# Kernel tuning notes

Hardware: AMD Instinct MI355X
Metric: run time of the kernel (lower is better)

Reference implementation:

```python
import jax, jax.numpy as jnp
import numpy as np

D_CONV = 4
D_STATE = 16
DT_RANK = 64


def _silu(x):
    return x * jax.nn.sigmoid(x)


def setup_inputs() -> dict:
    key = jax.random.key(0)
    ks = jax.random.split(key, 10)
    B, L, dim = 2, 1024, 1024
    d_inner = 2 * dim
    s = lambda fan: 1.0 / np.sqrt(fan)
    inp = {
        "x": jax.random.normal(ks[0], (B, L, dim), jnp.float32),
        "ln_w": jnp.ones((dim,), jnp.float32),
        "ln_b": jnp.zeros((dim,), jnp.float32),
        "w_in": jax.random.normal(ks[1], (2 * d_inner, dim), jnp.float32) * s(dim),
        "conv_w": jax.random.normal(ks[2], (d_inner, D_CONV), jnp.float32) * s(D_CONV),
        "conv_b": jnp.zeros((d_inner,), jnp.float32),
        "w_xproj": jax.random.normal(ks[3], (DT_RANK + 2 * D_STATE, d_inner), jnp.float32) * s(d_inner),
        "w_dt": jax.random.normal(ks[4], (d_inner, DT_RANK), jnp.float32) * s(DT_RANK),
        "b_dt": jax.random.normal(ks[5], (d_inner,), jnp.float32) * 0.1,
        # S4D-real init: A = -(1..d_state) per channel
        "a_log": jnp.tile(jnp.log(jnp.arange(1, D_STATE + 1, dtype=jnp.float32)), (d_inner, 1)),
        "d_skip": jnp.ones((d_inner,), jnp.float32),
        "w_out": jax.random.normal(ks[6], (dim, d_inner), jnp.float32) * s(d_inner),
    }
    return inp


def reference(x, ln_w, ln_b, w_in, conv_w, conv_b, w_xproj, w_dt, b_dt, a_log, d_skip, w_out):
    B, L, dim = x.shape
    residual = x

    # LayerNorm
    mu = jnp.mean(x, axis=-1, keepdims=True)
    var = jnp.mean((x - mu) ** 2, axis=-1, keepdims=True)
    xn = (x - mu) * jax.lax.rsqrt(var + 1e-5) * ln_w + ln_b

    # in_proj -> (x_ssm, z) each (B, L, d_inner)
    xz = jnp.einsum("bld,ed->ble", xn, w_in)
    d_inner = xz.shape[-1] // 2
    xs, z = xz[..., :d_inner], xz[..., d_inner:]

    # depthwise causal conv1d (kernel D_CONV) + SiLU
    xp = jnp.pad(xs, ((0, 0), (D_CONV - 1, 0), (0, 0)))
    xc = conv_b
    for k in range(D_CONV):
        xc = xc + conv_w[:, k] * xp[:, k : k + L, :]
    u = _silu(xc)  # (B, L, d_inner)

    # x_proj -> dt, B, C
    x_dbl = jnp.einsum("ble,re->blr", u, w_xproj)
    dt_r = x_dbl[..., :DT_RANK]
    B_ssm = x_dbl[..., DT_RANK : DT_RANK + D_STATE]         # (B, L, n)
    C_ssm = x_dbl[..., DT_RANK + D_STATE :]                 # (B, L, n)

    dt = jax.nn.softplus(jnp.einsum("blr,er->ble", dt_r, w_dt) + b_dt)  # (B, L, d_inner)

    A = -jnp.exp(a_log)  # (d_inner, n)
    deltaA = jnp.exp(jnp.einsum("ble,en->blen", dt, A))            # (B, L, e, n)
    deltaBu = jnp.einsum("ble,bln,ble->blen", dt, B_ssm, u)        # (B, L, e, n)

    # selective scan over L
    def step(h, ins):
        dA_t, dBu_t, C_t = ins
        h = dA_t * h + dBu_t                       # (B, e, n)
        y = jnp.einsum("ben,bn->be", h, C_t)
        return h, y

    h0 = jnp.zeros((B, d_inner, D_STATE), xs.dtype)
    _, ys = jax.lax.scan(
        step,
        h0,
        (deltaA.transpose(1, 0, 2, 3), deltaBu.transpose(1, 0, 2, 3), C_ssm.transpose(1, 0, 2)),
    )
    y = ys.transpose(1, 0, 2) + u * d_skip         # (B, L, e)

    y = y * _silu(z)
    out = jnp.einsum("ble,de->bld", y, w_out)
    return residual + out
```

## Files before the change

kernel.cpp:

```cpp
#include <hip/hip_runtime.h>
#include <hip/hip_bf16.h>


#define LC 16
#define NCHUNK 64

typedef short bf16x8 __attribute__((ext_vector_type(8)));
typedef float f32x4  __attribute__((ext_vector_type(4)));

static __device__ __forceinline__ float siluf(float x) { return x / (1.f + __expf(-x)); }
static __device__ __forceinline__ unsigned short f2bf(float f) {
    unsigned int u = __float_as_uint(f);
    unsigned int r = (u + 0x7fffu + ((u >> 16) & 1u)) >> 16;
    return (unsigned short)r;
}
static __device__ __forceinline__ float bfb(unsigned short u) {
    return __uint_as_float(((unsigned int)u) << 16);
}
static __device__ __forceinline__ void gload_lds16(const void* g, void* l) {
    __builtin_amdgcn_global_load_lds(
        (const __attribute__((address_space(1))) void*)g,
        (__attribute__((address_space(3))) void*)l, 16, 0, 0);
}

__global__ __launch_bounds__(256) void setup_kernel(
    const float* __restrict__ w_in,  unsigned short* __restrict__ w_in_b,
    const float* __restrict__ w_out, unsigned short* __restrict__ w_out_b,
    const float* __restrict__ w_dt,  unsigned short* __restrict__ w_dt_b,
    const float* __restrict__ x,
    const float* __restrict__ ln_w,
    const float* __restrict__ ln_b,
    unsigned short* __restrict__ xn)
{
    int bid = blockIdx.x, tid = threadIdx.x;
    if (bid < 6272) {
        int i = bid * 256 + tid;
        const float* in; unsigned short* outp; int j;
        if (i < 1048576)      { in = w_in;  outp = w_in_b;  j = i; }
        else if (i < 1572864) { in = w_out; outp = w_out_b; j = i - 1048576; }
        else if (i < 1605632) { in = w_dt;  outp = w_dt_b;  j = i - 1572864; }
        else return;
        float4 v = reinterpret_cast<const float4*>(in)[j];
        ushort4 o = { f2bf(v.x), f2bf(v.y), f2bf(v.z), f2bf(v.w) };
        reinterpret_cast<ushort4*>(outp)[j] = o;
        return;
    }
    int m = bid - 6272;
    const float4* xr = reinterpret_cast<const float4*>(x) + (size_t)m * 256;
    float4 r = xr[tid];
    float f0 = r.x, f1 = r.y, f2 = r.z, f3 = r.w;
    float s  = f0 + f1 + f2 + f3;
    float s2 = f0*f0 + f1*f1 + f2*f2 + f3*f3;
    #pragma unroll
    for (int off = 32; off > 0; off >>= 1) {
        s  += __shfl_down(s, off);
        s2 += __shfl_down(s2, off);
    }
    __shared__ float red[8];
    if ((tid & 63) == 0) { red[tid >> 6] = s; red[4 + (tid >> 6)] = s2; }
    __syncthreads();
    float st = red[0] + red[1] + red[2] + red[3];
    float qt = red[4] + red[5] + red[6] + red[7];
    float mu   = st * (1.f / 1024.f);
    float var  = qt * (1.f / 1024.f) - mu * mu;
    float rstd = rsqrtf(var + 1e-5f);
    float4 wv = reinterpret_cast<const float4*>(ln_w)[tid];
    float4 bv = reinterpret_cast<const float4*>(ln_b)[tid];
    ushort4 o = { f2bf((f0 - mu) * rstd * wv.x + bv.x),
                  f2bf((f1 - mu) * rstd * wv.y + bv.y),
                  f2bf((f2 - mu) * rstd * wv.z + bv.z),
                  f2bf((f3 - mu) * rstd * wv.w + bv.w) };
    reinterpret_cast<ushort4*>(xn + (size_t)m * 1024)[tid] = o;
}

__global__ __launch_bounds__(256) void gemm_bf16_nt(
    const unsigned short* __restrict__ A, int lda,
    const unsigned short* __restrict__ B, int ldb,
    int Kslice,
    float* __restrict__ C, unsigned short* __restrict__ Cb, int ldc,
    int ep, size_t Cstride)
{
    __shared__ short As[3 * 64 * 32];
    __shared__ short Bs[3 * 128 * 32];
    int tid = threadIdx.x;
    int z = blockIdx.z;
    A += (size_t)z * Kslice;
    B += (size_t)z * Kslice;
    C += (size_t)z * Cstride;

    int gx = gridDim.x;
    int wg = blockIdx.y * gx + blockIdx.x;
    int nwg = gx * gridDim.y;
    int cpx = nwg >> 3;
    int swz = (wg & 7) * cpx + (wg >> 3);
    int bx = swz % gx, by = swz / gx;

    int m0 = by * 64, n0 = bx * 128;
    int lane = tid & 63, wave = tid >> 6;
    int wm = (wave >> 1) * 32, wn = (wave & 1) * 64;
    int frow = lane & 15, fq = lane >> 4;

    f32x4 acc[2][4] = {};

    int lrow = lane >> 2;
    int scol = (lane & 3) * 8;
    const unsigned short* AgL = A + (size_t)(m0 + wave * 16 + lrow) * lda + scol;
    const unsigned short* BgL = B + (size_t)(n0 + wave * 16 + lrow) * ldb + scol;
    int aoff = (wave * 16) * 32;
    int boff = (wave * 16) * 32;

    #pragma unroll
    for (int p = 0; p < 2; ++p) {
        int nk = p * 32;
        gload_lds16(AgL + nk,                    As + p * 2048 + aoff);
        gload_lds16(BgL + nk,                    Bs + p * 4096 + boff);
        gload_lds16(BgL + (size_t)64 * ldb + nk, Bs + p * 4096 + boff + 64 * 32);
    }

    int cur = 0;
    for (int k0 = 0; k0 < Kslice; k0 += 32) {
        if (k0 + 32 < Kslice) {
            asm volatile("s_waitcnt vmcnt(3) lgkmcnt(0)" ::: "memory");
        } else {
            asm volatile("s_waitcnt vmcnt(0) lgkmcnt(0)" ::: "memory");
        }
        __builtin_amdgcn_s_barrier();
        int nk = k0 + 64;
        if (nk < Kslice) {
            int stg = cur - 1; if (stg < 0) stg = 2;
            gload_lds16(AgL + nk,                    As + stg * 2048 + aoff);
            gload_lds16(BgL + nk,                    Bs + stg * 4096 + boff);
            gload_lds16(BgL + (size_t)64 * ldb + nk, Bs + stg * 4096 + boff + 64 * 32);
        }
        const short* Ac = As + cur * 2048;
        const short* Bc = Bs + cur * 4096;
        bf16x8 af[2], bfr[4];
        #pragma unroll
        for (int i = 0; i < 2; ++i)
            af[i] = *reinterpret_cast<const bf16x8*>(Ac + (wm + i * 16 + frow) * 32 + fq * 8);
        #pragma unroll
        for (int j = 0; j < 4; ++j)
            bfr[j] = *reinterpret_cast<const bf16x8*>(Bc + (wn + j * 16 + frow) * 32 + fq * 8);
        #pragma unroll
        for (int i = 0; i < 2; ++i)
            #pragma unroll
            for (int j = 0; j < 4; ++j)
                acc[i][j] = __builtin_amdgcn_mfma_f32_16x16x32_bf16(af[i], bfr[j], acc[i][j], 0, 0, 0);
        cur = (cur == 2) ? 0 : cur + 1;
    }

    int cn = lane & 15, rq = (lane >> 4) * 4;
    #pragma unroll
    for (int i = 0; i < 2; ++i) {
        #pragma unroll
        for (int j = 0; j < 4; ++j) {
            #pragma unroll
            for (int r = 0; r < 4; ++r) {
                int row = m0 + wm + i * 16 + rq + r;
                int col = n0 + wn + j * 16 + cn;
                float v = acc[i][j][r];
                if (ep == 0) {
                    C[(size_t)row * ldc + col] = v;
                } else {
                    Cb[(size_t)row * ldc + col] = f2bf(v);
                }
            }
        }
    }
}

__global__ __launch_bounds__(256) void out_reduce(
    const float* __restrict__ part, const float* __restrict__ x,
    float* __restrict__ out)
{
    int i = blockIdx.x * 256 + threadIdx.x;
    float4 s = reinterpret_cast<const float4*>(x)[i];
    #pragma unroll
    for (int z = 0; z < 4; ++z) {
        float4 p = reinterpret_cast<const float4*>(part + (size_t)z * 2097152)[i];
        s.x += p.x; s.y += p.y; s.z += p.z; s.w += p.w;
    }
    reinterpret_cast<float4*>(out)[i] = s;
}

__global__ __launch_bounds__(256) void xproj_splitk(
    const unsigned short* __restrict__ xz,
    const float* __restrict__ cw,
    const float* __restrict__ cb,
    const float* __restrict__ B,
    unsigned short* __restrict__ u,
    float* __restrict__ part)
{
    __shared__ float As[16][68];
    __shared__ float Bs[16][100];
    int tid = threadIdx.x;
    int m0 = blockIdx.x * 64;
    int k0 = blockIdx.y * 64;
    int tx = tid & 15;
    int ty = tid >> 4;
    float acc[4][6] = {};
    int arow = tid >> 2, akg = (tid & 3) << 2;
    int brow1 = (256 + tid) >> 2, bkg1 = ((256 + tid) & 3) << 2;
    int m = m0 + arow;
    int l = m & 1023;

    for (int ks = 0; ks < 64; ks += 16) {
        int e0 = k0 + ks + akg;
        float xv[4][4];
        #pragma unroll
        for (int kk = 0; kk < 4; ++kk) {
            ushort4 t = make_ushort4(0, 0, 0, 0);
            if (l - 3 + kk >= 0)
                t = *reinterpret_cast<const ushort4*>(xz + (size_t)(m - 3 + kk) * 4096 + e0);
            xv[kk][0] = bfb(t.x); xv[kk][1] = bfb(t.y);
            xv[kk][2] = bfb(t.z); xv[kk][3] = bfb(t.w);
        }
        float4 cbv = *reinterpret_cast<const float4*>(cb + e0);
        float cbs[4] = { cbv.x, cbv.y, cbv.z, cbv.w };
        float res[4];
        #pragma unroll
        for (int j = 0; j < 4; ++j) {
            float4 w = *reinterpret_cast<const float4*>(cw + (size_t)(e0 + j) * 4);
            float a = cbs[j];
            a = fmaf(w.x, xv[0][j], a);
            a = fmaf(w.y, xv[1][j], a);
            a = fmaf(w.z, xv[2][j], a);
            a = fmaf(w.w, xv[3][j], a);
            res[j] = siluf(a);
        }
        ushort4 uo = { f2bf(res[0]), f2bf(res[1]), f2bf(res[2]), f2bf(res[3]) };
        *reinterpret_cast<ushort4*>(u + (size_t)m * 2048 + e0) = uo;

        float4 bv0 = make_float4(0.f, 0.f, 0.f, 0.f), bv1 = bv0;
        if (arow < 96)  bv0 = *reinterpret_cast<const float4*>(B + (size_t)arow * 2048 + k0 + ks + akg);
        if (brow1 < 96) bv1 = *reinterpret_cast<const float4*>(B + (size_t)brow1 * 2048 + k0 + ks + bkg1);
        __syncthreads();
        As[akg + 0][arow] = res[0]; As[akg + 1][arow] = res[1];
        As[akg + 2][arow] = res[2]; As[akg + 3][arow] = res[3];
        if (arow < 96) {
            Bs[akg + 0][arow] = bv0.x; Bs[akg + 1][arow] = bv0.y;
            Bs[akg + 2][arow] = bv0.z; Bs[akg + 3][arow] = bv0.w;
        }
        if (brow1 < 96) {
            Bs[bkg1 + 0][brow1] = bv1.x; Bs[bkg1 + 1][brow1] = bv1.y;
            Bs[bkg1 + 2][brow1] = bv1.z; Bs[bkg1 + 3][brow1] = bv1.w;
        }
        __syncthreads();
        #pragma unroll
        for (int k = 0; k < 16; ++k) {
            float aa[4], bb[6];
            #pragma unroll
            for (int i = 0; i < 4; ++i) aa[i] = As[k][ty * 4 + i];
            #pragma unroll
            for (int j = 0; j < 6; ++j) bb[j] = Bs[k][tx * 6 + j];
            #pragma unroll
            for (int i = 0; i < 4; ++i)
                #pragma unroll
                for (int j = 0; j < 6; ++j)
                    acc[i][j] = fmaf(aa[i], bb[j], acc[i][j]);
        }
    }
    float* p = part + (size_t)blockIdx.y * 196608;
    #pragma unroll
    for (int i = 0; i < 4; ++i)
        #pragma unroll
        for (int j = 0; j < 6; ++j)
            p[(size_t)(m0 + ty * 4 + i) * 96 + tx * 6 + j] = acc[i][j];
}

__global__ __launch_bounds__(256) void xproj_reduce(
    const float* __restrict__ part, float* __restrict__ xdbl)
{
    int i = blockIdx.x * 256 + threadIdx.x;
    float s = 0.f;
    #pragma unroll
    for (int sd = 0; sd < 32; ++sd) s += part[(size_t)sd * 196608 + i];
    xdbl[i] = s;
}

static __device__ __forceinline__ void dt_tile256(
    const float* __restrict__ xdbl, const unsigned short* __restrict__ w_dt_b,
    const float* __restrict__ b_dt, size_t rbase, int et,
    int lane, int wave, float dtl[LC][256])
{
    int frow = lane & 15, fq = lane >> 4;
    bf16x8 af[2];
    #pragma unroll
    for (int kk = 0; kk < 2; ++kk) {
        const float* ap = xdbl + (rbase + frow) * 96 + kk * 32 + fq * 8;
        float4 a0 = *reinterpret_cast<const float4*>(ap);
        float4 a1 = *reinterpret_cast<const float4*>(ap + 4);
        bf16x8 t;
        t[0] = (short)f2bf(a0.x); t[1] = (short)f2bf(a0.y);
        t[2] = (short)f2bf(a0.z); t[3] = (short)f2bf(a0.w);
        t[4] = (short)f2bf(a1.x); t[5] = (short)f2bf(a1.y);
        t[6] = (short)f2bf(a1.z); t[7] = (short)f2bf(a1.w);
        af[kk] = t;
    }
    f32x4 dacc[4] = {};
    #pragma unroll
    for (int j = 0; j < 4; ++j)
        #pragma unroll
        for (int kk = 0; kk < 2; ++kk) {
            int row_e = et * 256 + wave * 64 + j * 16 + frow;
            bf16x8 bfr = *reinterpret_cast<const bf16x8*>(
                w_dt_b + (size_t)row_e * 64 + kk * 32 + fq * 8);
            dacc[j] = __builtin_amdgcn_mfma_f32_16x16x32_bf16(af[kk], bfr, dacc[j], 0, 0, 0);
        }
    int cn = lane & 15, rq = (lane >> 4) * 4;
    #pragma unroll
    for (int j = 0; j < 4; ++j)
        #pragma unroll
        for (int r = 0; r < 4; ++r) {
            int lrow = rq + r;
            int ecol = wave * 64 + j * 16 + cn;
            float v = dacc[j][r] + b_dt[et * 256 + ecol];
            v = (v > 20.f) ? v : log1pf(__expf(v));
            dtl[lrow][ecol] = bfb(f2bf(v));
        }
}

__global__ __launch_bounds__(256) void scan_part1(
    const unsigned short* __restrict__ u,
    const float* __restrict__ xdbl,
    const unsigned short* __restrict__ w_dt_b,
    const float* __restrict__ b_dt,
    const float* __restrict__ a_log,
    float* __restrict__ hpart,
    float* __restrict__ Aprod)
{
    __shared__ float dtl[LC][256];
    int tid = threadIdx.x;
    int lane = tid & 63, wave = tid >> 6;
    int bid = blockIdx.x;
    int c = bid & 63, et = (bid >> 6) & 7, b = bid >> 9;
    int e = et * 256 + tid;
    size_t rbase = (size_t)b * 1024 + c * LC;

    dt_tile256(xdbl, w_dt_b, b_dt, rbase, et, lane, wave, dtl);

    float A[16];
    #pragma unroll
    for (int q = 0; q < 4; ++q) {
        float4 al = *reinterpret_cast<const float4*>(a_log + (size_t)e * 16 + q * 4);
        A[q * 4 + 0] = -__expf(al.x); A[q * 4 + 1] = -__expf(al.y);
        A[q * 4 + 2] = -__expf(al.z); A[q * 4 + 3] = -__expf(al.w);
    }
    float h[16], P[16];
    #pragma unroll
    for (int n = 0; n < 16; ++n) { h[n] = 0.f; P[n] = 1.f; }

    const unsigned short* u_p = u + rbase * 2048 + e;
    const float* b_p = xdbl + rbase * 96 + 64;
    __syncthreads();
    #pragma unroll
    for (int l = 0; l < LC; ++l) {
        float dtv = dtl[l][tid];
        float u_c = bfb(u_p[(size_t)l * 2048]);
        float Bv[16];
        #pragma unroll
        for (int q = 0; q < 4; ++q) {
            float4 bv = *reinterpret_cast<const float4*>(b_p + (size_t)l * 96 + q * 4);
            Bv[q * 4 + 0] = bv.x; Bv[q * 4 + 1] = bv.y;
            Bv[q * 4 + 2] = bv.z; Bv[q * 4 + 3] = bv.w;
        }
        float du = dtv * u_c;
        #pragma unroll
        for (int n = 0; n < 16; ++n) {
            float d = __expf(dtv * A[n]);
            h[n] = fmaf(d, h[n], du * Bv[n]);
            P[n] *= d;
        }
    }
    size_t oidx = (size_t)c * 65536 + ((size_t)b * 2048 + e) * 16;
    #pragma unroll
    for (int q = 0; q < 4; ++q) {
        *reinterpret_cast<float4*>(hpart + oidx + q * 4) =
            make_float4(h[q * 4], h[q * 4 + 1], h[q * 4 + 2], h[q * 4 + 3]);
        *reinterpret_cast<float4*>(Aprod + oidx + q * 4) =
            make_float4(P[q * 4], P[q * 4 + 1], P[q * 4 + 2], P[q * 4 + 3]);
    }
}

__global__ __launch_bounds__(256) void scan_combine(
    const float* __restrict__ hpart,
    const float* __restrict__ Aprod,
    float* __restrict__ hinit)
{
    int t = blockIdx.x * 256 + threadIdx.x;
    float h = 0.f;
    #pragma unroll 8
    for (int c = 0; c < NCHUNK; ++c) {
        hinit[(size_t)c * 65536 + t] = h;
        float P  = Aprod[(size_t)c * 65536 + t];
        float hp = hpart[(size_t)c * 65536 + t];
        h = fmaf(P, h, hp);
    }
}

__global__ __launch_bounds__(256) void scan_part2(
    const unsigned short* __restrict__ u,
    const float* __restrict__ xdbl,
    const unsigned short* __restrict__ w_dt_b,
    const float* __restrict__ b_dt,
    const unsigned short* __restrict__ xz,
    const float* __restrict__ a_log,
    const float* __restrict__ d_skip,
    const float* __restrict__ hinit,
    unsigned short* __restrict__ y)
{
    __shared__ float dtl[LC][256];
    int tid = threadIdx.x;
    int lane = tid & 63, wave = tid >> 6;
    int bid = blockIdx.x;
    int c = bid & 63, et = (bid >> 6) & 7, b = bid >> 9;
    int e = et * 256 + tid;
    size_t rbase = (size_t)b * 1024 + c * LC;

    dt_tile256(xdbl, w_dt_b, b_dt, rbase, et, lane, wave, dtl);

    float A[16];
    #pragma unroll
    for (int q = 0; q < 4; ++q) {
        float4 al = *reinterpret_cast<const float4*>(a_log + (size_t)e * 16 + q * 4);
        A[q * 4 + 0] = -__expf(al.x); A[q * 4 + 1] = -__expf(al.y);
        A[q * 4 + 2] = -__expf(al.z); A[q * 4 + 3] = -__expf(al.w);
    }
    float dsk = d_skip[e];
    float h[16];
    size_t oidx = (size_t)c * 65536 + ((size_t)b * 2048 + e) * 16;
    #pragma unroll
    for (int q = 0; q < 4; ++q) {
        float4 hq = *reinterpret_cast<const float4*>(hinit + oidx + q * 4);
        h[q * 4 + 0] = hq.x; h[q * 4 + 1] = hq.y;
        h[q * 4 + 2] = hq.z; h[q * 4 + 3] = hq.w;
    }

    const unsigned short* u_p = u + rbase * 2048 + e;
    const unsigned short* z_p = xz + rbase * 4096 + 2048 + e;
    const float* b_p = xdbl + rbase * 96 + 64;
    unsigned short* y_p = y + rbase * 2048 + e;
    __syncthreads();
    #pragma unroll
    for (int l = 0; l < LC; ++l) {
        float dtv = dtl[l][tid];
        float u_c = bfb(u_p[(size_t)l * 2048]);
        float Bv[16], Cv[16];
        #pragma unroll
        for (int q = 0; q < 4; ++q) {
            float4 bv = *reinterpret_cast<const float4*>(b_p + (size_t)l * 96 + q * 4);
            float4 cv = *reinterpret_cast<const float4*>(b_p + (size_t)l * 96 + 16 + q * 4);
            Bv[q * 4 + 0] = bv.x; Bv[q * 4 + 1] = bv.y;
            Bv[q * 4 + 2] = bv.z; Bv[q * 4 + 3] = bv.w;
            Cv[q * 4 + 0] = cv.x; Cv[q * 4 + 1] = cv.y;
            Cv[q * 4 + 2] = cv.z; Cv[q * 4 + 3] = cv.w;
        }
        float du = dtv * u_c;
        float p = 0.f;
        #pragma unroll
        for (int n = 0; n < 16; ++n) {
            float d = __expf(dtv * A[n]);
            h[n] = fmaf(d, h[n], du * Bv[n]);
            p = fmaf(h[n], Cv[n], p);
        }
        float zv = bfb(z_p[(size_t)l * 4096]);
        y_p[(size_t)l * 2048] = f2bf((p + u_c * dsk) * siluf(zv));
    }
}

extern "C" void kernel_launch(void* const* d_in, const int* in_sizes, int n_in,
                              void* d_out, int out_size, void* d_ws, size_t ws_size,
                              hipStream_t stream) {
    const float* x       = (const float*)d_in[0];
    const float* ln_w    = (const float*)d_in[1];
    const float* ln_b    = (const float*)d_in[2];
    const float* w_in    = (const float*)d_in[3];
    const float* conv_w  = (const float*)d_in[4];
    const float* conv_b  = (const float*)d_in[5];
    const float* w_xproj = (const float*)d_in[6];
    const float* w_dt    = (const float*)d_in[7];
    const float* b_dt    = (const float*)d_in[8];
    const float* a_log   = (const float*)d_in[9];
    const float* d_skip  = (const float*)d_in[10];
    const float* w_out   = (const float*)d_in[11];
    float* out = (float*)d_out;

    float* ws = (float*)d_ws;
    unsigned short* xn_b    = (unsigned short*)(ws);
    unsigned short* xz_b    = (unsigned short*)(ws + 1048576);
    unsigned short* u_b     = (unsigned short*)(ws + 5242880);
    float* xdbl  = ws + 7340032;
    float* hpart = ws + 9633792;
    float* Aprod = ws + 13828096;
    float* hinit = ws + 18022400;
    unsigned short* y_b     = (unsigned short*)(ws + 22216704);
    unsigned short* w_in_b  = (unsigned short*)(ws + 24313856);
    unsigned short* w_out_b = (unsigned short*)(ws + 26411008);
    unsigned short* w_dt_b  = (unsigned short*)(ws + 27459584);
    float* xpart = ws + 9633792;
    float* opart = ws + 1048576;

    setup_kernel<<<8320, 256, 0, stream>>>(w_in, w_in_b, w_out, w_out_b, w_dt, w_dt_b,
                                           x, ln_w, ln_b, xn_b);
    gemm_bf16_nt<<<dim3(32, 32, 1), 256, 0, stream>>>(xn_b, 1024, w_in_b, 1024, 1024,
                                                      nullptr, xz_b, 4096, 3, 0);
    xproj_splitk<<<dim3(32, 32), 256, 0, stream>>>(xz_b, conv_w, conv_b, w_xproj,
                                                   u_b, xpart);
    xproj_reduce<<<768, 256, 0, stream>>>(xpart, xdbl);
    scan_part1<<<1024, 256, 0, stream>>>(u_b, xdbl, w_dt_b, b_dt, a_log, hpart, Aprod);
    scan_combine<<<256, 256, 0, stream>>>(hpart, Aprod, hinit);
    scan_part2<<<1024, 256, 0, stream>>>(u_b, xdbl, w_dt_b, b_dt, xz_b, a_log,
                                         d_skip, hinit, y_b);
    gemm_bf16_nt<<<dim3(8, 32, 4), 256, 0, stream>>>(y_b, 2048, w_out_b, 2048, 512,
                                                     opart, nullptr, 1024, 0, 2097152);
    out_reduce<<<2048, 256, 0, stream>>>(opart, x, out);
}
```

Baseline: 278.1 us.

## Split SSM state across thread pairs and double scan chunk length

Result: slower. 288.5 us (+3.7%).

```diff
diff --git a/kernel.cpp b/kernel.cpp
--- a/kernel.cpp
+++ b/kernel.cpp
@@ -2,8 +2,8 @@
 #include <hip/hip_bf16.h>
 
 
-#define LC 16
-#define NCHUNK 64
+#define LC 32
+#define NCHUNK 32
 
 typedef short bf16x8 __attribute__((ext_vector_type(8)));
 typedef float f32x4  __attribute__((ext_vector_type(4)));
@@ -278,46 +278,52 @@
     xdbl[i] = s;
 }
 
-static __device__ __forceinline__ void dt_tile256(
+static __device__ __forceinline__ void dt_tile128(
     const float* __restrict__ xdbl, const unsigned short* __restrict__ w_dt_b,
     const float* __restrict__ b_dt, size_t rbase, int et,
-    int lane, int wave, float dtl[LC][256])
+    int lane, int wave, float dtl[LC][128])
 {
     int frow = lane & 15, fq = lane >> 4;
-    bf16x8 af[2];
-    #pragma unroll
-    for (int kk = 0; kk < 2; ++kk) {
-        const float* ap = xdbl + (rbase + frow) * 96 + kk * 32 + fq * 8;
-        float4 a0 = *reinterpret_cast<const float4*>(ap);
-        float4 a1 = *reinterpret_cast<const float4*>(ap + 4);
-        bf16x8 t;
-        t[0] = (short)f2bf(a0.x); t[1] = (short)f2bf(a0.y);
-        t[2] = (short)f2bf(a0.z); t[3] = (short)f2bf(a0.w);
-        t[4] = (short)f2bf(a1.x); t[5] = (short)f2bf(a1.y);
-        t[6] = (short)f2bf(a1.z); t[7] = (short)f2bf(a1.w);
-        af[kk] = t;
-    }
-    f32x4 dacc[4] = {};
-    #pragma unroll
-    for (int j = 0; j < 4; ++j)
+    bf16x8 af[2][2];
+    #pragma unroll
+    for (int i = 0; i < 2; ++i)
         #pragma unroll
         for (int kk = 0; kk < 2; ++kk) {
-            int row_e = et * 256 + wave * 64 + j * 16 + frow;
+            const float* ap = xdbl + (rbase + i * 16 + frow) * 96 + kk * 32 + fq * 8;
+            float4 a0 = *reinterpret_cast<const float4*>(ap);
+            float4 a1 = *reinterpret_cast<const float4*>(ap + 4);
+            bf16x8 t;
+            t[0] = (short)f2bf(a0.x); t[1] = (short)f2bf(a0.y);
+            t[2] = (short)f2bf(a0.z); t[3] = (short)f2bf(a0.w);
+            t[4] = (short)f2bf(a1.x); t[5] = (short)f2bf(a1.y);
+            t[6] = (short)f2bf(a1.z); t[7] = (short)f2bf(a1.w);
+            af[i][kk] = t;
+        }
+    f32x4 dacc[2][2] = {};
+    #pragma unroll
+    for (int j = 0; j < 2; ++j)
+        #pragma unroll
+        for (int kk = 0; kk < 2; ++kk) {
+            int row_e = et * 128 + wave * 32 + j * 16 + frow;
             bf16x8 bfr = *reinterpret_cast<const bf16x8*>(
                 w_dt_b + (size_t)row_e * 64 + kk * 32 + fq * 8);
-            dacc[j] = __builtin_amdgcn_mfma_f32_16x16x32_bf16(af[kk], bfr, dacc[j], 0, 0, 0);
+            #pragma unroll
+            for (int i = 0; i < 2; ++i)
+                dacc[i][j] = __builtin_amdgcn_mfma_f32_16x16x32_bf16(af[i][kk], bfr, dacc[i][j], 0, 0, 0);
         }
     int cn = lane & 15, rq = (lane >> 4) * 4;
     #pragma unroll
-    for (int j = 0; j < 4; ++j)
-        #pragma unroll
-        for (int r = 0; r < 4; ++r) {
-            int lrow = rq + r;
-            int ecol = wave * 64 + j * 16 + cn;
-            float v = dacc[j][r] + b_dt[et * 256 + ecol];
-            v = (v > 20.f) ? v : log1pf(__expf(v));
-            dtl[lrow][ecol] = bfb(f2bf(v));
-        }
+    for (int i = 0; i < 2; ++i)
+        #pragma unroll
+        for (int j = 0; j < 2; ++j)
+            #pragma unroll
+            for (int r = 0; r < 4; ++r) {
+                int row = i * 16 + rq + r;
+                int col = wave * 32 + j * 16 + cn;
+                float v = dacc[i][j][r] + b_dt[et * 128 + col];
+                v = (v > 20.f) ? v : log1pf(__expf(v));
+                dtl[row][col] = bfb(f2bf(v));
+            }
 }
 
 __global__ __launch_bounds__(256) void scan_part1(
@@ -329,57 +335,54 @@
     float* __restrict__ hpart,
     float* __restrict__ Aprod)
 {
-    __shared__ float dtl[LC][256];
+    __shared__ float dtl[LC][128];
     int tid = threadIdx.x;
     int lane = tid & 63, wave = tid >> 6;
     int bid = blockIdx.x;
-    int c = bid & 63, et = (bid >> 6) & 7, b = bid >> 9;
-    int e = et * 256 + tid;
+    int c = bid & 31, et = (bid >> 5) & 15, b = bid >> 9;
+    int ch = tid >> 1, ng = tid & 1;
+    int e = et * 128 + ch;
     size_t rbase = (size_t)b * 1024 + c * LC;
 
-    dt_tile256(xdbl, w_dt_b, b_dt, rbase, et, lane, wave, dtl);
-
-    float A[16];
-    #pragma unroll
-    for (int q = 0; q < 4; ++q) {
-        float4 al = *reinterpret_cast<const float4*>(a_log + (size_t)e * 16 + q * 4);
-        A[q * 4 + 0] = -__expf(al.x); A[q * 4 + 1] = -__expf(al.y);
-        A[q * 4 + 2] = -__expf(al.z); A[q * 4 + 3] = -__expf(al.w);
-    }
-    float h[16], P[16];
-    #pragma unroll
-    for (int n = 0; n < 16; ++n) { h[n] = 0.f; P[n] = 1.f; }
+    dt_tile128(xdbl, w_dt_b, b_dt, rbase, et, lane, wave, dtl);
+
+    const float L2E = 1.4426950408889634f;
+    float A2[8];
+    {
+        float4 a0 = *reinterpret_cast<const float4*>(a_log + (size_t)e * 16 + ng * 8);
+        float4 a1 = *reinterpret_cast<const float4*>(a_log + (size_t)e * 16 + ng * 8 + 4);
+        A2[0] = -__expf(a0.x) * L2E; A2[1] = -__expf(a0.y) * L2E;
+        A2[2] = -__expf(a0.z) * L2E; A2[3] = -__expf(a0.w) * L2E;
+        A2[4] = -__expf(a1.x) * L2E; A2[5] = -__expf(a1.y) * L2E;
+        A2[6] = -__expf(a1.z) * L2E; A2[7] = -__expf(a1.w) * L2E;
+    }
+    float h[8], P[8];
+    #pragma unroll
+    for (int n = 0; n < 8; ++n) { h[n] = 0.f; P[n] = 1.f; }
 
     const unsigned short* u_p = u + rbase * 2048 + e;
-    const float* b_p = xdbl + rbase * 96 + 64;
+    const float* b_p = xdbl + rbase * 96 + 64 + ng * 8;
     __syncthreads();
-    #pragma unroll
+    #pragma unroll 8
     for (int l = 0; l < LC; ++l) {
-        float dtv = dtl[l][tid];
+        float dtv = dtl[l][ch];
         float u_c = bfb(u_p[(size_t)l * 2048]);
-        float Bv[16];
-        #pragma unroll
-        for (int q = 0; q < 4; ++q) {
-            float4 bv = *reinterpret_cast<const float4*>(b_p + (size_t)l * 96 + q * 4);
-            Bv[q * 4 + 0] = bv.x; Bv[q * 4 + 1] = bv.y;
-            Bv[q * 4 + 2] = bv.z; Bv[q * 4 + 3] = bv.w;
-        }
+        float4 b0 = *reinterpret_cast<const float4*>(b_p + (size_t)l * 96);
+        float4 b1 = *reinterpret_cast<const float4*>(b_p + (size_t)l * 96 + 4);
+        float Bv[8] = { b0.x, b0.y, b0.z, b0.w, b1.x, b1.y, b1.z, b1.w };
         float du = dtv * u_c;
         #pragma unroll
-        for (int n = 0; n < 16; ++n) {
-            float d = __expf(dtv * A[n]);
+        for (int n = 0; n < 8; ++n) {
+            float d = exp2f(dtv * A2[n]);
             h[n] = fmaf(d, h[n], du * Bv[n]);
             P[n] *= d;
         }
     }
-    size_t oidx = (size_t)c * 65536 + ((size_t)b * 2048 + e) * 16;
-    #pragma unroll
-    for (int q = 0; q < 4; ++q) {
-        *reinterpret_cast<float4*>(hpart + oidx + q * 4) =
-            make_float4(h[q * 4], h[q * 4 + 1], h[q * 4 + 2], h[q * 4 + 3]);
-        *reinterpret_cast<float4*>(Aprod + oidx + q * 4) =
-            make_float4(P[q * 4], P[q * 4 + 1], P[q * 4 + 2], P[q * 4 + 3]);
-    }
+    size_t oidx = (size_t)c * 65536 + ((size_t)b * 2048 + e) * 16 + ng * 8;
+    *reinterpret_cast<float4*>(hpart + oidx)     = make_float4(h[0], h[1], h[2], h[3]);
+    *reinterpret_cast<float4*>(hpart + oidx + 4) = make_float4(h[4], h[5], h[6], h[7]);
+    *reinterpret_cast<float4*>(Aprod + oidx)     = make_float4(P[0], P[1], P[2], P[3]);
+    *reinterpret_cast<float4*>(Aprod + oidx + 4) = make_float4(P[4], P[5], P[6], P[7]);
 }
 
 __global__ __launch_bounds__(256) void scan_combine(
@@ -409,62 +412,65 @@
     const float* __restrict__ hinit,
     unsigned short* __restrict__ y)
 {
-    __shared__ float dtl[LC][256];
+    __shared__ float dtl[LC][128];
     int tid = threadIdx.x;
     int lane = tid & 63, wave = tid >> 6;
     int bid = blockIdx.x;
-    int c = bid & 63, et = (bid >> 6) & 7, b = bid >> 9;
-    int e = et * 256 + tid;
+    int c = bid & 31, et = (bid >> 5) & 15, b = bid >> 9;
+    int ch = tid >> 1, ng = tid & 1;
+    int e = et * 128 + ch;
     size_t rbase = (size_t)b * 1024 + c * LC;
 
-    dt_tile256(xdbl, w_dt_b, b_dt, rbase, et, lane, wave, dtl);
-
-    float A[16];
-    #pragma unroll
-    for (int q = 0; q < 4; ++q) {
-        float4 al = *reinterpret_cast<const float4*>(a_log + (size_t)e * 16 + q * 4);
-        A[q * 4 + 0] = -__expf(al.x); A[q * 4 + 1] = -__expf(al.y);
-        A[q * 4 + 2] = -__expf(al.z); A[q * 4 + 3] = -__expf(al.w);
+    dt_tile128(xdbl, w_dt_b, b_dt, rbase, et, lane, wave, dtl);
+
+    const float L2E = 1.4426950408889634f;
+    float A2[8];
+    {
+        float4 a0 = *reinterpret_cast<const float4*>(a_log + (size_t)e * 16 + ng * 8);
+        float4 a1 = *reinterpret_cast<const float4*>(a_log + (size_t)e * 16 + ng * 8 + 4);
+        A2[0] = -__expf(a0.x) * L2E; A2[1] = -__expf(a0.y) * L2E;
+        A2[2] = -__expf(a0.z) * L2E; A2[3] = -__expf(a0.w) * L2E;
+        A2[4] = -__expf(a1.x) * L2E; A2[5] = -__expf(a1.y) * L2E;
+        A2[6] = -__expf(a1.z) * L2E; A2[7] = -__expf(a1.w) * L2E;
     }
     float dsk = d_skip[e];
-    float h[16];
-    size_t oidx = (size_t)c * 65536 + ((size_t)b * 2048 + e) * 16;
-    #pragma unroll
-    for (int q = 0; q < 4; ++q) {
-        float4 hq = *reinterpret_cast<const float4*>(hinit + oidx + q * 4);
-        h[q * 4 + 0] = hq.x; h[q * 4 + 1] = hq.y;
-        h[q * 4 + 2] = hq.z; h[q * 4 + 3] = hq.w;
+    float h[8];
+    size_t oidx = (size_t)c * 65536 + ((size_t)b * 2048 + e) * 16 + ng * 8;
+    {
+        float4 h0 = *reinterpret_cast<const float4*>(hinit + oidx);
+        float4 h1 = *reinterpret_cast<const float4*>(hinit + oidx + 4);
+        h[0] = h0.x; h[1] = h0.y; h[2] = h0.z; h[3] = h0.w;
+        h[4] = h1.x; h[5] = h1.y; h[6] = h1.z; h[7] = h1.w;
     }
 
     const unsigned short* u_p = u + rbase * 2048 + e;
     const unsigned short* z_p = xz + rbase * 4096 + 2048 + e;
-    const float* b_p = xdbl + rbase * 96 + 64;
+    const float* b_p = xdbl + rbase * 96 + 64 + ng * 8;
     unsigned short* y_p = y + rbase * 2048 + e;
     __syncthreads();
-    #pragma unroll
+    #pragma unroll 8
     for (int l = 0; l < LC; ++l) {
-        float dtv = dtl[l][tid];
+        float dtv = dtl[l][ch];
         float u_c = bfb(u_p[(size_t)l * 2048]);
-        float Bv[16], Cv[16];
-        #pragma unroll
-        for (int q = 0; q < 4; ++q) {
-            float4 bv = *reinterpret_cast<const float4*>(b_p + (size_t)l * 96 + q * 4);
-            float4 cv = *reinterpret_cast<const float4*>(b_p + (size_t)l * 96 + 16 + q * 4);
-            Bv[q * 4 + 0] = bv.x; Bv[q * 4 + 1] = bv.y;
-            Bv[q * 4 + 2] = bv.z; Bv[q * 4 + 3] = bv.w;
-            Cv[q * 4 + 0] = cv.x; Cv[q * 4 + 1] = cv.y;
-            Cv[q * 4 + 2] = cv.z; Cv[q * 4 + 3] = cv.w;
-        }
+        float4 b0 = *reinterpret_cast<const float4*>(b_p + (size_t)l * 96);
+        float4 b1 = *reinterpret_cast<const float4*>(b_p + (size_t)l * 96 + 4);
+        float4 c0 = *reinterpret_cast<const float4*>(b_p + (size_t)l * 96 + 16);
+        float4 c1 = *reinterpret_cast<const float4*>(b_p + (size_t)l * 96 + 20);
+        float Bv[8] = { b0.x, b0.y, b0.z, b0.w, b1.x, b1.y, b1.z, b1.w };
+        float Cv[8] = { c0.x, c0.y, c0.z, c0.w, c1.x, c1.y, c1.z, c1.w };
         float du = dtv * u_c;
         float p = 0.f;
         #pragma unroll
-        for (int n = 0; n < 16; ++n) {
-            float d = __expf(dtv * A[n]);
+        for (int n = 0; n < 8; ++n) {
+            float d = exp2f(dtv * A2[n]);
             h[n] = fmaf(d, h[n], du * Bv[n]);
             p = fmaf(h[n], Cv[n], p);
         }
-        float zv = bfb(z_p[(size_t)l * 4096]);
-        y_p[(size_t)l * 2048] = f2bf((p + u_c * dsk) * siluf(zv));
+        p += __shfl_xor(p, 1);
+        if (ng == 0) {
+            float zv = bfb(z_p[(size_t)l * 4096]);
+            y_p[(size_t)l * 2048] = f2bf((p + u_c * dsk) * siluf(zv));
+        }
     }
 }
 
```
